# Kernel tuning notes

Hardware: AMD Instinct MI355X
Metric: run time of the kernel (lower is better)

Reference implementation:

```python
import jax, jax.numpy as jnp
import numpy as np

VOCAB = 50257
EMBED = 128
B, S = 64, 4096


def setup_inputs() -> dict:
    key = jax.random.key(0)
    k1, k2, k3 = jax.random.split(key, 3)
    x = jax.random.randint(k1, (B, S), 0, VOCAB)
    # Linear(n_symboles, output_size) weight has shape [output_size, n_symboles]
    W = jax.random.normal(k2, (EMBED, VOCAB), dtype=jnp.float32) * 0.02
    b = jax.random.normal(k3, (EMBED,), dtype=jnp.float32) * 0.02
    return {"x": x, "W": W, "b": b}


def reference(x, W, b):
    # one_hot(x, V) @ W.T + b  ==  gather rows of W.T at x, then add bias.
    # Mathematically identical to the torch one-hot + Linear path, but
    # avoids materializing the [B, S, V] one-hot tensor.
    return W.T[x] + b  # [B, S, EMBED]
```

## Files before the change

kernel.cpp:

```cpp
#include <hip/hip_runtime.h>

#define VOCAB 50257
#define EMBED 128
#define NTOK  (64 * 4096)

typedef float    f32x4 __attribute__((ext_vector_type(4)));
typedef _Float16 f16x8 __attribute__((ext_vector_type(8)));

__global__ void transpose_h_kernel(const float* __restrict__ W,
                                   _Float16* __restrict__ Wt) {
    __shared__ float tile[64][65];
    const int t  = threadIdx.x;
    const int v0 = blockIdx.x * 64;
    const int e0 = blockIdx.y * 64;
    const bool full = (v0 + 64 <= VOCAB);

    if (full) {
#pragma unroll
        for (int it = 0; it < 4; ++it) {
            const int e_loc = (t >> 4) + it * 16;
            const int c4    = (t & 15) * 4;
            f32x4 val = *(const f32x4*)&W[(size_t)(e0 + e_loc) * VOCAB + v0 + c4];
            tile[c4 + 0][e_loc] = val.x;
            tile[c4 + 1][e_loc] = val.y;
            tile[c4 + 2][e_loc] = val.z;
            tile[c4 + 3][e_loc] = val.w;
        }
    } else {
#pragma unroll
        for (int it = 0; it < 16; ++it) {
            const int e_loc = (t >> 6) + it * 4;
            const int c     = t & 63;
            const int v     = v0 + c;
            tile[c][e_loc] = (v < VOCAB) ? W[(size_t)(e0 + e_loc) * VOCAB + v]
                                         : 0.0f;
        }
    }
    __syncthreads();

#pragma unroll
    for (int it = 0; it < 2; ++it) {
        const int v_loc = (t >> 3) + it * 32;
        const int eo    = (t & 7) * 8;
        const int v     = v0 + v_loc;
        if (v < VOCAB) {
            f16x8 h;
#pragma unroll
            for (int j = 0; j < 8; ++j)
                h[j] = (_Float16)tile[v_loc][eo + j];
            *(f16x8*)&Wt[(size_t)v * EMBED + e0 + eo] = h;
        }
    }
}

__global__ void gather_h_kernel(const int* __restrict__ x,
                                const f16x8* __restrict__ Wt,
                                const float* __restrict__ bias,
                                f32x4* __restrict__ out) {
    const int gid    = blockIdx.x * blockDim.x + threadIdx.x;
    const int stride = gridDim.x * blockDim.x;
    const int oct    = gid & 15;
    const f32x4 blo  = *(const f32x4*)&bias[oct * 8];
    const f32x4 bhi  = *(const f32x4*)&bias[oct * 8 + 4];

    const int t0 = gid >> 4;
    const int t1 = (gid + stride) >> 4;
    const int i0 = x[t0];
    const int i1 = x[t1];
    const f16x8 h0 = Wt[i0 * 16 + oct];
    const f16x8 h1 = Wt[i1 * 16 + oct];

    f32x4 lo, hi;
    lo.x = (float)h0[0] + blo.x; lo.y = (float)h0[1] + blo.y;
    lo.z = (float)h0[2] + blo.z; lo.w = (float)h0[3] + blo.w;
    hi.x = (float)h0[4] + bhi.x; hi.y = (float)h0[5] + bhi.y;
    hi.z = (float)h0[6] + bhi.z; hi.w = (float)h0[7] + bhi.w;
    f32x4* o0 = out + (size_t)t0 * 32 + oct * 2;
    o0[0] = lo; o0[1] = hi;

    lo.x = (float)h1[0] + blo.x; lo.y = (float)h1[1] + blo.y;
    lo.z = (float)h1[2] + blo.z; lo.w = (float)h1[3] + blo.w;
    hi.x = (float)h1[4] + bhi.x; hi.y = (float)h1[5] + bhi.y;
    hi.z = (float)h1[6] + bhi.z; hi.w = (float)h1[7] + bhi.w;
    f32x4* o1 = out + (size_t)t1 * 32 + oct * 2;
    o1[0] = lo; o1[1] = hi;
}

__global__ void direct_kernel(const int* __restrict__ x,
                              const float* __restrict__ W,
                              const float* __restrict__ bias,
                              f32x4* __restrict__ out) {
    const int gid   = blockIdx.x * blockDim.x + threadIdx.x;
    const int token = gid >> 5;
    const int e4    = gid & 31;
    const int idx   = x[token];
    const int e     = e4 * 4;
    f32x4 r;
    r.x = W[(size_t)(e + 0) * VOCAB + idx] + bias[e + 0];
    r.y = W[(size_t)(e + 1) * VOCAB + idx] + bias[e + 1];
    r.z = W[(size_t)(e + 2) * VOCAB + idx] + bias[e + 2];
    r.w = W[(size_t)(e + 3) * VOCAB + idx] + bias[e + 3];
    out[(size_t)token * 32 + e4] = r;
}

extern "C" void kernel_launch(void* const* d_in, const int* in_sizes, int n_in,
                              void* d_out, int out_size, void* d_ws, size_t ws_size,
                              hipStream_t stream) {
    const int*   x    = (const int*)d_in[0];
    const float* W    = (const float*)d_in[1];
    const float* bias = (const float*)d_in[2];

    const size_t wt_bytes = (size_t)VOCAB * EMBED * sizeof(_Float16);

    if (ws_size >= wt_bytes) {
        _Float16* Wt = (_Float16*)d_ws;
        dim3 tgrid((VOCAB + 63) / 64, 2);
        transpose_h_kernel<<<tgrid, 256, 0, stream>>>(W, Wt);

        const int gblocks = (NTOK * 16 / 2) / 256;
        gather_h_kernel<<<gblocks, 256, 0, stream>>>(x, (const f16x8*)Wt,
                                                     bias, (f32x4*)d_out);
    } else {
        const int dblocks = (NTOK * 32) / 256;
        direct_kernel<<<dblocks, 256, 0, stream>>>(x, W, bias, (f32x4*)d_out);
    }
}
```

Measured before the change: 47.75 us.

## Fold bias into fp16 transposed table and restructure gather to four items per thread

Adds the bias during the transpose pass, so the fp16 table already holds W^T+b and the gather kernel no longer loads or adds bias. The gather kernel now gives each thread four independent 8-byte fp16x4 loads with 16-byte fp32 stores instead of two 16-byte loads, aiming for more memory-level parallelism and coalesced writes. Rounding the bias-added value to fp16 changes precision slightly compared with adding the bias in fp32.

```diff
diff --git a/kernel.cpp b/kernel.cpp
--- a/kernel.cpp
+++ b/kernel.cpp
@@ -5,9 +5,11 @@
 #define NTOK  (64 * 4096)
 
 typedef float    f32x4 __attribute__((ext_vector_type(4)));
+typedef _Float16 f16x4 __attribute__((ext_vector_type(4)));
 typedef _Float16 f16x8 __attribute__((ext_vector_type(8)));
 
 __global__ void transpose_h_kernel(const float* __restrict__ W,
+                                   const float* __restrict__ bias,
                                    _Float16* __restrict__ Wt) {
     __shared__ float tile[64][65];
     const int t  = threadIdx.x;
@@ -38,52 +40,53 @@
     }
     __syncthreads();
 
+    const int eo = (t & 7) * 8;
+    const f32x4 ba = *(const f32x4*)&bias[e0 + eo];
+    const f32x4 bb = *(const f32x4*)&bias[e0 + eo + 4];
 #pragma unroll
     for (int it = 0; it < 2; ++it) {
         const int v_loc = (t >> 3) + it * 32;
-        const int eo    = (t & 7) * 8;
         const int v     = v0 + v_loc;
         if (v < VOCAB) {
             f16x8 h;
-#pragma unroll
-            for (int j = 0; j < 8; ++j)
-                h[j] = (_Float16)tile[v_loc][eo + j];
+            h[0] = (_Float16)(tile[v_loc][eo + 0] + ba.x);
+            h[1] = (_Float16)(tile[v_loc][eo + 1] + ba.y);
+            h[2] = (_Float16)(tile[v_loc][eo + 2] + ba.z);
+            h[3] = (_Float16)(tile[v_loc][eo + 3] + ba.w);
+            h[4] = (_Float16)(tile[v_loc][eo + 4] + bb.x);
+            h[5] = (_Float16)(tile[v_loc][eo + 5] + bb.y);
+            h[6] = (_Float16)(tile[v_loc][eo + 6] + bb.z);
+            h[7] = (_Float16)(tile[v_loc][eo + 7] + bb.w);
             *(f16x8*)&Wt[(size_t)v * EMBED + e0 + eo] = h;
         }
     }
 }
 
 __global__ void gather_h_kernel(const int* __restrict__ x,
-                                const f16x8* __restrict__ Wt,
-                                const float* __restrict__ bias,
+                                const f16x4* __restrict__ Wt,
                                 f32x4* __restrict__ out) {
     const int gid    = blockIdx.x * blockDim.x + threadIdx.x;
     const int stride = gridDim.x * blockDim.x;
-    const int oct    = gid & 15;
-    const f32x4 blo  = *(const f32x4*)&bias[oct * 8];
-    const f32x4 bhi  = *(const f32x4*)&bias[oct * 8 + 4];
 
-    const int t0 = gid >> 4;
-    const int t1 = (gid + stride) >> 4;
-    const int i0 = x[t0];
-    const int i1 = x[t1];
-    const f16x8 h0 = Wt[i0 * 16 + oct];
-    const f16x8 h1 = Wt[i1 * 16 + oct];
-
-    f32x4 lo, hi;
-    lo.x = (float)h0[0] + blo.x; lo.y = (float)h0[1] + blo.y;
-    lo.z = (float)h0[2] + blo.z; lo.w = (float)h0[3] + blo.w;
-    hi.x = (float)h0[4] + bhi.x; hi.y = (float)h0[5] + bhi.y;
-    hi.z = (float)h0[6] + bhi.z; hi.w = (float)h0[7] + bhi.w;
-    f32x4* o0 = out + (size_t)t0 * 32 + oct * 2;
-    o0[0] = lo; o0[1] = hi;
-
-    lo.x = (float)h1[0] + blo.x; lo.y = (float)h1[1] + blo.y;
-    lo.z = (float)h1[2] + blo.z; lo.w = (float)h1[3] + blo.w;
-    hi.x = (float)h1[4] + bhi.x; hi.y = (float)h1[5] + bhi.y;
-    hi.z = (float)h1[6] + bhi.z; hi.w = (float)h1[7] + bhi.w;
-    f32x4* o1 = out + (size_t)t1 * 32 + oct * 2;
-    o1[0] = lo; o1[1] = hi;
+    int g[4], idx[4];
+#pragma unroll
+    for (int k = 0; k < 4; ++k) {
+        g[k]   = gid + k * stride;
+        idx[k] = x[g[k] >> 5];
+    }
+    f16x4 h[4];
+#pragma unroll
+    for (int k = 0; k < 4; ++k)
+        h[k] = Wt[(size_t)idx[k] * 32 + (g[k] & 31)];
+#pragma unroll
+    for (int k = 0; k < 4; ++k) {
+        f32x4 r;
+        r.x = (float)h[k][0];
+        r.y = (float)h[k][1];
+        r.z = (float)h[k][2];
+        r.w = (float)h[k][3];
+        out[g[k]] = r;
+    }
 }
 
 __global__ void direct_kernel(const int* __restrict__ x,
@@ -115,11 +118,11 @@
     if (ws_size >= wt_bytes) {
         _Float16* Wt = (_Float16*)d_ws;
         dim3 tgrid((VOCAB + 63) / 64, 2);
-        transpose_h_kernel<<<tgrid, 256, 0, stream>>>(W, Wt);
+        transpose_h_kernel<<<tgrid, 256, 0, stream>>>(W, bias, Wt);
 
-        const int gblocks = (NTOK * 16 / 2) / 256;
-        gather_h_kernel<<<gblocks, 256, 0, stream>>>(x, (const f16x8*)Wt,
-                                                     bias, (f32x4*)d_out);
+        const int gblocks = (NTOK * 32 / 4) / 256;
+        gather_h_kernel<<<gblocks, 256, 0, stream>>>(x, (const f16x4*)Wt,
+                                                     (f32x4*)d_out);
     } else {
         const int dblocks = (NTOK * 32) / 256;
         direct_kernel<<<dblocks, 256, 0, stream>>>(x, W, bias, (f32x4*)d_out);
```

Result: no change. 46.94 us (-1.7%).
